# Performance work log

Hardware: AMD Instinct MI355X
Metric: run time of the kernel (lower is better)

## Reference

```python
import jax, jax.numpy as jnp
import numpy as np

VOCAB, EMB, HID, FC1, NCLS = 32000, 2048, 2048, 256, 3
T, B = 256, 128


def setup_inputs() -> dict:
    key = jax.random.key(0)
    ks = jax.random.split(key, 10)
    s_e = 1.0  # torch Embedding default init N(0,1)
    s_h = 1.0 / np.sqrt(HID)
    s_f1 = 1.0 / np.sqrt(HID)
    s_f2 = 1.0 / np.sqrt(FC1)
    return {
        "x": jax.random.randint(ks[0], (T, B), 0, VOCAB, dtype=jnp.int64)
        if jax.config.jax_enable_x64 else jax.random.randint(ks[0], (T, B), 0, VOCAB, dtype=jnp.int32),
        "emb": jax.random.normal(ks[1], (VOCAB, EMB), dtype=jnp.float32) * s_e,
        "W_ih": jax.random.uniform(ks[2], (HID, EMB), jnp.float32, -s_h, s_h),
        "W_hh": jax.random.uniform(ks[3], (HID, HID), jnp.float32, -s_h, s_h),
        "b_ih": jax.random.uniform(ks[4], (HID,), jnp.float32, -s_h, s_h),
        "b_hh": jax.random.uniform(ks[5], (HID,), jnp.float32, -s_h, s_h),
        "fc1_w": jax.random.uniform(ks[6], (FC1, HID), jnp.float32, -s_f1, s_f1),
        "fc1_b": jax.random.uniform(ks[7], (FC1,), jnp.float32, -s_f1, s_f1),
        "fc2_w": jax.random.uniform(ks[8], (NCLS, FC1), jnp.float32, -s_f2, s_f2),
        "fc2_b": jax.random.uniform(ks[9], (NCLS,), jnp.float32, -s_f2, s_f2),
    }


def reference(x, emb, W_ih, W_hh, b_ih, b_hh, fc1_w, fc1_b, fc2_w, fc2_b):
    # Embedding: [T, B] -> [T, B, E]
    xe = emb[x]
    # Precompute input projections for all steps in one big GEMM: [T, B, H]
    xproj = jnp.einsum("tbe,he->tbh", xe, W_ih) + b_ih + b_hh
    h0 = jnp.zeros((x.shape[1], W_hh.shape[0]), dtype=xe.dtype)

    def step(h, xp_t):
        h = jnp.tanh(xp_t + h @ W_hh.T)
        return h, None

    h_last, _ = jax.lax.scan(step, h0, xproj)
    # MLP head: hidden -> 256 -> relu -> 3
    z = jax.nn.relu(h_last @ fc1_w.T + fc1_b)
    return z @ fc2_w.T + fc2_b
```

## Files before the change

kernel.cpp:

```cpp
#include <hip/hip_runtime.h>

typedef _Float16 half8 __attribute__((ext_vector_type(8)));
typedef _Float16 half4v __attribute__((ext_vector_type(4)));
typedef float float4v __attribute__((ext_vector_type(4)));

#define HID 2048
#define EMBD 2048
#define BATCH 128
#define TSTEPS 256
#define STEP ((size_t)BATCH * HID)

__global__ __launch_bounds__(256) void cast_f16_kernel(const float* __restrict__ src,
                                                       _Float16* __restrict__ dst, int n) {
    int i = (blockIdx.x * 256 + threadIdx.x) * 4;
    int stride = gridDim.x * 256 * 4;
    for (; i < n; i += stride) {
        float4v v = *(const float4v*)(src + i);
        half4v h;
        h[0] = (_Float16)v[0]; h[1] = (_Float16)v[1];
        h[2] = (_Float16)v[2]; h[3] = (_Float16)v[3];
        *(half4v*)(dst + i) = h;
    }
}

__global__ __launch_bounds__(256) void bias_kernel(const float* __restrict__ a,
                                                   const float* __restrict__ b,
                                                   float* __restrict__ dst) {
    int i = blockIdx.x * 256 + threadIdx.x;
    if (i < HID) dst[i] = a[i] + b[i];
}

__global__ __launch_bounds__(256) void phaseA_kernel(const int* __restrict__ x,
                                                     const float* __restrict__ emb,
                                                     const _Float16* __restrict__ w16,
                                                     const float* __restrict__ bias,
                                                     _Float16* __restrict__ xproj) {
    __shared__ __align__(16) _Float16 As[128 * 64];
    __shared__ __align__(16) _Float16 Bs[128 * 64];

    const int tid = threadIdx.x;
    const int bx  = blockIdx.x;
    const int nt = bx & 15, mt = bx >> 4;
    const long m0 = (long)mt * 128;
    const long n0 = (long)nt * 128;
    const int lane = tid & 63, w = tid >> 6;
    const int ln15 = lane & 15, kg = lane >> 4;
    const int wr = (w >> 1) * 64, wc = (w & 1) * 64;

    int xr[4];
#pragma unroll
    for (int it = 0; it < 4; ++it) xr[it] = x[m0 + ((it * 256 + tid) >> 3)];

    float4v acc[4][4];
#pragma unroll
    for (int m = 0; m < 4; ++m)
#pragma unroll
        for (int n = 0; n < 4; ++n) acc[m][n] = (float4v){0.f, 0.f, 0.f, 0.f};

    for (int kt = 0; kt < 32; ++kt) {
        __syncthreads();
#pragma unroll
        for (int it = 0; it < 4; ++it) {
            int c = it * 256 + tid;
            const float* src = emb + (long)xr[it] * EMBD + kt * 64 + (c & 7) * 8;
            float4v v0 = *(const float4v*)src;
            float4v v1 = *(const float4v*)(src + 4);
            half8 hv;
#pragma unroll
            for (int q = 0; q < 4; ++q) { hv[q] = (_Float16)v0[q]; hv[4 + q] = (_Float16)v1[q]; }
            *(half8*)(&As[c * 8]) = hv;
        }
#pragma unroll
        for (int it = 0; it < 4; ++it) {
            int c = it * 256 + tid;
            const _Float16* src = w16 + (n0 + (c >> 3)) * (long)EMBD + kt * 64 + (c & 7) * 8;
            *(half8*)(&Bs[c * 8]) = *(const half8*)src;
        }
        __syncthreads();
#pragma unroll
        for (int kk = 0; kk < 2; ++kk) {
            half8 a[4], b[4];
#pragma unroll
            for (int m = 0; m < 4; ++m)
                a[m] = *(half8*)(&As[(wr + m * 16 + ln15) * 64 + kk * 32 + kg * 8]);
#pragma unroll
            for (int n = 0; n < 4; ++n)
                b[n] = *(half8*)(&Bs[(wc + n * 16 + ln15) * 64 + kk * 32 + kg * 8]);
#pragma unroll
            for (int m = 0; m < 4; ++m)
#pragma unroll
                for (int n = 0; n < 4; ++n)
                    acc[m][n] = __builtin_amdgcn_mfma_f32_16x16x32_f16(b[n], a[m], acc[m][n], 0, 0, 0);
        }
    }
#pragma unroll
    for (int m = 0; m < 4; ++m) {
        long mg = m0 + wr + m * 16 + ln15;
#pragma unroll
        for (int n = 0; n < 4; ++n) {
            int nb = (int)n0 + wc + n * 16 + kg * 4;
            float4v bv = *(const float4v*)(bias + nb);
            union { half4v h; unsigned long long u; } pk;
#pragma unroll
            for (int r = 0; r < 4; ++r) pk.h[r] = (_Float16)(acc[m][n][r] + bv[r]);
            *(unsigned long long*)(xproj + mg * HID + nb) = pk.u;
        }
    }
}

__global__ __launch_bounds__(256, 1) void scan_kernel(_Float16* __restrict__ xb,
                                                      const _Float16* __restrict__ whh,
                                                      float* __restrict__ hlast,
                                                      unsigned* __restrict__ flags) {
    __shared__ __align__(16) _Float16 Wl[32 * 2048];
    __shared__ float part[4][16 * 33];

    const int tid = threadIdx.x;
    const int bx = blockIdx.x;
    const int gid = bx & 3, sub = bx >> 2;
    const int m0 = gid * 32, n0 = sub * 32;
    const int lane = tid & 63, w = tid >> 6;
    const int ln15 = lane & 15, kg = lane >> 4;
    const int pr = w >> 1, kh = w & 1;

    for (int it = 0; it < 32; ++it) {
        int c = it * 256 + tid;
        int col = c >> 8, ch = c & 255;
        half8 v = *(const half8*)(whh + (long)(n0 + col) * HID + ch * 8);
        *(half8*)((char*)Wl + col * 4096 + ((ch * 16) ^ ((col & 7) << 4))) = v;
    }
    __syncthreads();

    unsigned* gfl = flags + gid * 64;
    const unsigned long long* gfl64 = (const unsigned long long*)gfl;
    const size_t arow = (size_t)(m0 + pr * 16 + ln15);
    const int wb0 = ln15 * 4096, wb1 = (16 + ln15) * 4096;
    const int swz = (ln15 & 7) << 4;
    const int kb = kh * 2048;
    const int rp = tid >> 7, ridx = tid & 127;
    const int rrow = ridx >> 3, rc4 = (ridx & 7) * 4;
    const size_t oidx = (size_t)(m0 + rp * 16 + rrow) * HID + n0 + rc4;

    for (int s = 0; s < TSTEPS; ++s) {
        unsigned long long xbits = __hip_atomic_load(
            (const unsigned long long*)(xb + (size_t)(s + 1) * STEP + oidx),
            __ATOMIC_RELAXED, __HIP_MEMORY_SCOPE_AGENT);

        float4v acc0 = (float4v){0.f, 0.f, 0.f, 0.f};
        float4v acc1 = (float4v){0.f, 0.f, 0.f, 0.f};
        if (s > 0) {
            for (;;) {
                bool ok = true;
                if (lane < 32) {
                    unsigned long long v = __hip_atomic_load(gfl64 + lane,
                                            __ATOMIC_RELAXED, __HIP_MEMORY_SCOPE_AGENT);
                    ok = ((unsigned)v >= (unsigned)s) && ((unsigned)(v >> 32) >= (unsigned)s);
                }
                if (__all(ok)) break;
                __builtin_amdgcn_s_sleep(2);
            }
            asm volatile("" ::: "memory");
            __builtin_amdgcn_sched_barrier(0);

            const _Float16* hrow = xb + (size_t)(s - 1) * STEP + arow * HID + kh * 1024;
#pragma unroll
            for (int j = 0; j < 32; ++j) {
                half8 a = *(const half8*)(hrow + j * 32 + kg * 8);
                int k2 = kb + j * 64 + kg * 16;
                half8 b0 = *(half8*)((char*)Wl + wb0 + (k2 ^ swz));
                half8 b1 = *(half8*)((char*)Wl + wb1 + (k2 ^ swz));
                acc0 = __builtin_amdgcn_mfma_f32_16x16x32_f16(a, b0, acc0, 0, 0, 0);
                acc1 = __builtin_amdgcn_mfma_f32_16x16x32_f16(a, b1, acc1, 0, 0, 0);
            }
#pragma unroll
            for (int r = 0; r < 4; ++r) {
                part[w][(kg * 4 + r) * 33 + ln15] = acc0[r];
                part[w][(kg * 4 + r) * 33 + 16 + ln15] = acc1[r];
            }
        }

        float s0 = 0.f, s1 = 0.f, s2 = 0.f, s3 = 0.f;
        if (s > 0) {
            __syncthreads();
            const float* p0 = &part[2 * rp][rrow * 33 + rc4];
            const float* p1 = &part[2 * rp + 1][rrow * 33 + rc4];
            s0 = p0[0] + p1[0]; s1 = p0[1] + p1[1];
            s2 = p0[2] + p1[2]; s3 = p0[3] + p1[3];
        }
        union { unsigned long long u; half4v h; } xbv; xbv.u = xbits;
        float o0 = tanhf(s0 + (float)xbv.h[0]);
        float o1 = tanhf(s1 + (float)xbv.h[1]);
        float o2 = tanhf(s2 + (float)xbv.h[2]);
        float o3 = tanhf(s3 + (float)xbv.h[3]);

        if (s < TSTEPS - 1) {
            union { half4v h; unsigned long long u; } pk;
            pk.h[0] = (_Float16)o0; pk.h[1] = (_Float16)o1;
            pk.h[2] = (_Float16)o2; pk.h[3] = (_Float16)o3;
            __hip_atomic_store((unsigned long long*)(xb + (size_t)s * STEP + oidx),
                               pk.u, __ATOMIC_RELAXED, __HIP_MEMORY_SCOPE_AGENT);
            __syncthreads();
            if (tid == 0)
                __hip_atomic_store(&gfl[sub], (unsigned)(s + 1),
                                   __ATOMIC_RELAXED, __HIP_MEMORY_SCOPE_AGENT);
        } else {
            float4v f = {o0, o1, o2, o3};
            *(float4v*)(hlast + oidx) = f;
        }
    }
}

__global__ __launch_bounds__(64) void fc1_kernel(const float* __restrict__ hlast,
                                                 const float* __restrict__ w,
                                                 const float* __restrict__ b,
                                                 float* __restrict__ z) {
    int bb = blockIdx.x;
    int j = blockIdx.y * 64 + threadIdx.x;
    const float* hr = hlast + (long)bb * HID;
    const float* wr = w + (long)j * HID;
    float acc = 0.f;
    for (int k = 0; k < HID; k += 4) {
        float4v hv = *(const float4v*)(hr + k);
        float4v wv = *(const float4v*)(wr + k);
        acc += hv[0] * wv[0] + hv[1] * wv[1] + hv[2] * wv[2] + hv[3] * wv[3];
    }
    acc += b[j];
    z[bb * 256 + j] = fmaxf(acc, 0.f);
}

__global__ __launch_bounds__(256) void fc2_kernel(const float* __restrict__ z,
                                                  const float* __restrict__ w,
                                                  const float* __restrict__ b,
                                                  float* __restrict__ out) {
    __shared__ float red[4];
    int bb = blockIdx.x;
    int tid = threadIdx.x;
    float zv = z[bb * 256 + tid];
    for (int c = 0; c < 3; ++c) {
        float s = zv * w[c * 256 + tid];
        for (int off = 32; off > 0; off >>= 1) s += __shfl_down(s, off, 64);
        if ((tid & 63) == 0) red[tid >> 6] = s;
        __syncthreads();
        if (tid == 0) out[bb * 3 + c] = red[0] + red[1] + red[2] + red[3] + b[c];
        __syncthreads();
    }
}

extern "C" void kernel_launch(void* const* d_in, const int* in_sizes, int n_in,
                              void* d_out, int out_size, void* d_ws, size_t ws_size,
                              hipStream_t stream) {
    const int*   x    = (const int*)d_in[0];
    const float* emb  = (const float*)d_in[1];
    const float* Wih  = (const float*)d_in[2];
    const float* Whh  = (const float*)d_in[3];
    const float* bih  = (const float*)d_in[4];
    const float* bhh  = (const float*)d_in[5];
    const float* fc1w = (const float*)d_in[6];
    const float* fc1b = (const float*)d_in[7];
    const float* fc2w = (const float*)d_in[8];
    const float* fc2b = (const float*)d_in[9];
    float* out = (float*)d_out;

    char* ws = (char*)d_ws;
    size_t off = 0;
    _Float16* xb    = (_Float16*)(ws + off); off += 257 * STEP * 2;
    _Float16* wih16 = (_Float16*)(ws + off); off += (size_t)HID * EMBD * 2;
    _Float16* whh16 = (_Float16*)(ws + off); off += (size_t)HID * HID * 2;
    float*    bias  = (float*)(ws + off);    off += (size_t)HID * 4;
    float*    hlast = (float*)(ws + off);    off += (size_t)BATCH * HID * 4;
    float*    z     = (float*)(ws + off);    off += (size_t)BATCH * 256 * 4;
    unsigned* flags = (unsigned*)(ws + off); off += 4 * 64 * 4;

    hipMemsetAsync(flags, 0, 4 * 64 * 4, stream);

    cast_f16_kernel<<<4096, 256, 0, stream>>>(Wih, wih16, HID * EMBD);
    cast_f16_kernel<<<4096, 256, 0, stream>>>(Whh, whh16, HID * HID);
    bias_kernel<<<8, 256, 0, stream>>>(bih, bhh, bias);

    phaseA_kernel<<<4096, 256, 0, stream>>>(x, emb, wih16, bias, xb + STEP);

    void* args[] = {(void*)&xb, (void*)&whh16, (void*)&hlast, (void*)&flags};
    hipLaunchCooperativeKernel((const void*)scan_kernel, dim3(256), dim3(256), args, 0, stream);

    fc1_kernel<<<dim3(128, 4), 64, 0, stream>>>(hlast, fc1w, fc1b, z);
    fc2_kernel<<<BATCH, 256, 0, stream>>>(z, fc2w, fc2b, out);
}
```

Before: 2.532 ms.

## Pack scan sync flags into bytes, drop poll sleep, use direct-to-LDS loads

The per-step inter-block flags become single bytes, so one wavefront checks a group's 64 flags with 8 lanes of 64-bit loads and a SWAR zero-byte test, and the sleep in the spin loop is removed. This targets the barrier latency between the 256 sequential recurrence steps, at the cost of more memory polling traffic. The input-projection GEMM now loads weight tiles straight into LDS with global_load_lds. The fc1 head is rewritten to stage 8 batch rows in shared memory and reuse each weight row across them.

```diff
diff --git a/kernel.cpp b/kernel.cpp
--- a/kernel.cpp
+++ b/kernel.cpp
@@ -74,7 +74,9 @@
         for (int it = 0; it < 4; ++it) {
             int c = it * 256 + tid;
             const _Float16* src = w16 + (n0 + (c >> 3)) * (long)EMBD + kt * 64 + (c & 7) * 8;
-            *(half8*)(&Bs[c * 8]) = *(const half8*)src;
+            __builtin_amdgcn_global_load_lds((const __attribute__((address_space(1))) void*)src,
+                                             (__attribute__((address_space(3))) void*)&Bs[c * 8],
+                                             16, 0, 0);
         }
         __syncthreads();
 #pragma unroll
@@ -111,7 +113,7 @@
 __global__ __launch_bounds__(256, 1) void scan_kernel(_Float16* __restrict__ xb,
                                                       const _Float16* __restrict__ whh,
                                                       float* __restrict__ hlast,
-                                                      unsigned* __restrict__ flags) {
+                                                      unsigned char* __restrict__ flags) {
     __shared__ __align__(16) _Float16 Wl[32 * 2048];
     __shared__ float part[4][16 * 33];
 
@@ -131,7 +133,7 @@
     }
     __syncthreads();
 
-    unsigned* gfl = flags + gid * 64;
+    unsigned char* gfl = flags + gid * 64;
     const unsigned long long* gfl64 = (const unsigned long long*)gfl;
     const size_t arow = (size_t)(m0 + pr * 16 + ln15);
     const int wb0 = ln15 * 4096, wb1 = (16 + ln15) * 4096;
@@ -149,15 +151,17 @@
         float4v acc0 = (float4v){0.f, 0.f, 0.f, 0.f};
         float4v acc1 = (float4v){0.f, 0.f, 0.f, 0.f};
         if (s > 0) {
+            unsigned long long pat =
+                (unsigned long long)(unsigned char)(s - 1) * 0x0101010101010101ull;
             for (;;) {
                 bool ok = true;
-                if (lane < 32) {
+                if (lane < 8) {
                     unsigned long long v = __hip_atomic_load(gfl64 + lane,
                                             __ATOMIC_RELAXED, __HIP_MEMORY_SCOPE_AGENT);
-                    ok = ((unsigned)v >= (unsigned)s) && ((unsigned)(v >> 32) >= (unsigned)s);
+                    unsigned long long xx = v ^ pat;
+                    ok = !((xx - 0x0101010101010101ull) & ~xx & 0x8080808080808080ull);
                 }
                 if (__all(ok)) break;
-                __builtin_amdgcn_s_sleep(2);
             }
             asm volatile("" ::: "memory");
             __builtin_amdgcn_sched_barrier(0);
@@ -201,7 +205,7 @@
                                pk.u, __ATOMIC_RELAXED, __HIP_MEMORY_SCOPE_AGENT);
             __syncthreads();
             if (tid == 0)
-                __hip_atomic_store(&gfl[sub], (unsigned)(s + 1),
+                __hip_atomic_store(&gfl[sub], (unsigned char)(s + 1),
                                    __ATOMIC_RELAXED, __HIP_MEMORY_SCOPE_AGENT);
         } else {
             float4v f = {o0, o1, o2, o3};
@@ -210,22 +214,39 @@
     }
 }
 
-__global__ __launch_bounds__(64) void fc1_kernel(const float* __restrict__ hlast,
-                                                 const float* __restrict__ w,
-                                                 const float* __restrict__ b,
-                                                 float* __restrict__ z) {
-    int bb = blockIdx.x;
-    int j = blockIdx.y * 64 + threadIdx.x;
-    const float* hr = hlast + (long)bb * HID;
+__global__ __launch_bounds__(256) void fc1_kernel(const float* __restrict__ hlast,
+                                                  const float* __restrict__ w,
+                                                  const float* __restrict__ b,
+                                                  float* __restrict__ z) {
+    __shared__ float hs[8][256];
+    const int blk = blockIdx.x;
+    const int j = threadIdx.x;
+    const int bb0 = blk * 8;
+    float acc[8];
+#pragma unroll
+    for (int r = 0; r < 8; ++r) acc[r] = 0.f;
     const float* wr = w + (long)j * HID;
-    float acc = 0.f;
-    for (int k = 0; k < HID; k += 4) {
-        float4v hv = *(const float4v*)(hr + k);
-        float4v wv = *(const float4v*)(wr + k);
-        acc += hv[0] * wv[0] + hv[1] * wv[1] + hv[2] * wv[2] + hv[3] * wv[3];
-    }
-    acc += b[j];
-    z[bb * 256 + j] = fmaxf(acc, 0.f);
+    const int sr = j >> 5, sc = (j & 31) * 8;
+
+    for (int kt = 0; kt < 8; ++kt) {
+        __syncthreads();
+        float4v h0 = *(const float4v*)(hlast + (long)(bb0 + sr) * HID + kt * 256 + sc);
+        float4v h1 = *(const float4v*)(hlast + (long)(bb0 + sr) * HID + kt * 256 + sc + 4);
+        *(float4v*)&hs[sr][sc] = h0;
+        *(float4v*)&hs[sr][sc + 4] = h1;
+        __syncthreads();
+        for (int k = 0; k < 256; k += 4) {
+            float4v wv = *(const float4v*)(wr + kt * 256 + k);
+#pragma unroll
+            for (int r = 0; r < 8; ++r) {
+                float4v hv = *(const float4v*)&hs[r][k];
+                acc[r] += hv[0] * wv[0] + hv[1] * wv[1] + hv[2] * wv[2] + hv[3] * wv[3];
+            }
+        }
+    }
+    float bj = b[j];
+#pragma unroll
+    for (int r = 0; r < 8; ++r) z[(bb0 + r) * 256 + j] = fmaxf(acc[r] + bj, 0.f);
 }
 
 __global__ __launch_bounds__(256) void fc2_kernel(const float* __restrict__ z,
@@ -269,9 +290,9 @@
     float*    bias  = (float*)(ws + off);    off += (size_t)HID * 4;
     float*    hlast = (float*)(ws + off);    off += (size_t)BATCH * HID * 4;
     float*    z     = (float*)(ws + off);    off += (size_t)BATCH * 256 * 4;
-    unsigned* flags = (unsigned*)(ws + off); off += 4 * 64 * 4;
-
-    hipMemsetAsync(flags, 0, 4 * 64 * 4, stream);
+    unsigned char* flags = (unsigned char*)(ws + off); off += 256;
+
+    hipMemsetAsync(flags, 0, 256, stream);
 
     cast_f16_kernel<<<4096, 256, 0, stream>>>(Wih, wih16, HID * EMBD);
     cast_f16_kernel<<<4096, 256, 0, stream>>>(Whh, whh16, HID * HID);
@@ -282,6 +303,6 @@
     void* args[] = {(void*)&xb, (void*)&whh16, (void*)&hlast, (void*)&flags};
     hipLaunchCooperativeKernel((const void*)scan_kernel, dim3(256), dim3(256), args, 0, stream);
 
-    fc1_kernel<<<dim3(128, 4), 64, 0, stream>>>(hlast, fc1w, fc1b, z);
+    fc1_kernel<<<16, 256, 0, stream>>>(hlast, fc1w, fc1b, z);
     fc2_kernel<<<BATCH, 256, 0, stream>>>(z, fc2w, fc2b, out);
 }
```

Measured after the change: 2.731 ms. 7.9% more time.
